# Kernel tuning notes

Hardware: AMD Instinct MI355X
Metric: run time of the kernel (lower is better)

## Reference

```python
import jax, jax.numpy as jnp
import numpy as np
from jax import lax

B, H, W, C, G, K = 2, 64, 64, 256, 8, 9
CQ = C // 4  # PConv partial channels
HC = C // G  # head channels
PTS = np.array([[-1, -1], [-1, 0], [-1, 1], [0, -1], [0, 0], [0, 1],
                [1, -1], [1, 0], [1, 1]], np.float32)  # (K,2) as (dx,dy)


def setup_inputs() -> dict:
    key = jax.random.key(0)
    ks = jax.random.split(key, 13)
    n = lambda i, shp, s: jax.random.normal(ks[i], shp, jnp.float32) * s
    return {
        'x': jax.random.normal(ks[0], (B, H, W, C), jnp.float32),
        'qkv_w': n(1, (C, 3 * C), C ** -0.5),
        'qkv_b': n(2, (3 * C,), 0.02),
        'dw_w': n(3, (3, 3, 1, 3 * C), 1.0 / 3.0),
        'dw_b': n(4, (3 * C,), 0.02),
        'off_pconv_w': n(5, (G, CQ, CQ, 3, 3), (CQ * 9) ** -0.5),
        'off_w': n(6, (G, 2 * K, C), 0.1 * C ** -0.5),
        'off_b': n(7, (G, 2 * K), 0.1),
        'mask_pconv_w': n(8, (CQ, CQ, 3, 3), (CQ * 9) ** -0.5),
        'mask_w': n(9, (K, C), C ** -0.5),
        'mask_b': n(10, (K,), 0.02),
        'proj_w': n(11, (C, C), C ** -0.5),
        'proj_b': n(12, (C,), 0.02),
    }


def _dwconv_nhwc(x, w, b):
    # depthwise 3x3, pad 1, stride 1; x (B,H,W,ch), w (3,3,1,ch)
    ch = x.shape[-1]
    y = lax.conv_general_dilated(x, w, (1, 1), 'SAME',
                                 dimension_numbers=('NHWC', 'HWIO', 'NHWC'),
                                 feature_group_count=ch)
    return y + b


def _pconv_nchw(x, w):
    # partial conv: 3x3 (no bias) on first CQ channels, rest untouched
    dc = w.shape[0]
    x1 = lax.conv_general_dilated(x[:, :dc], w, (1, 1), 'SAME',
                                  dimension_numbers=('NCHW', 'OIHW', 'NCHW'))
    return jnp.concatenate([x1, x[:, dc:]], axis=1)


def _flow_warp(x, flow):
    # x (N,Cc,Hh,Ww), flow (N,2K,Hh,Ww) -> (N,Cc,K,Hh,Ww)
    # bilinear grid_sample, border padding, align_corners=True == sampling at
    # absolute pixel coords with coordinate clamping.
    N, Cc, Hh, Ww = x.shape
    Kk = flow.shape[1] // 2
    fl = flow.reshape(N, Kk, 2, Hh, Ww).transpose(0, 3, 4, 1, 2)  # (N,H,W,K,2)
    gy, gx = jnp.meshgrid(jnp.arange(Hh, dtype=x.dtype),
                          jnp.arange(Ww, dtype=x.dtype), indexing='ij')
    base = jnp.stack([gx, gy], axis=-1)  # (H,W,2) in (x,y) order
    coords = base[None, :, :, None, :] + fl  # (N,H,W,K,2)
    cx = jnp.clip(coords[..., 0], 0.0, Ww - 1)
    cy = jnp.clip(coords[..., 1], 0.0, Hh - 1)
    x0 = jnp.floor(cx)
    y0 = jnp.floor(cy)
    wx = (cx - x0).reshape(N, 1, -1)
    wy = (cy - y0).reshape(N, 1, -1)
    x0i = x0.astype(jnp.int32)
    y0i = y0.astype(jnp.int32)
    x1i = jnp.minimum(x0i + 1, Ww - 1)
    y1i = jnp.minimum(y0i + 1, Hh - 1)
    xf = x.reshape(N, Cc, Hh * Ww)

    def gather(yi, xi):
        idx = (yi * Ww + xi).reshape(N, -1)  # (N, H*W*K)
        return jax.vmap(lambda im, ix: im[:, ix])(xf, idx)  # (N,Cc,H*W*K)

    v00 = gather(y0i, x0i)
    v01 = gather(y0i, x1i)
    v10 = gather(y1i, x0i)
    v11 = gather(y1i, x1i)
    out = (v00 * (1 - wx) * (1 - wy) + v01 * wx * (1 - wy)
           + v10 * (1 - wx) * wy + v11 * wx * wy)
    return out.reshape(N, Cc, Hh, Ww, Kk).transpose(0, 1, 4, 2, 3)


def reference(x, qkv_w, qkv_b, dw_w, dw_b, off_pconv_w, off_w, off_b,
              mask_pconv_w, mask_w, mask_b, proj_w, proj_b):
    Bb, Hh, Ww, Cc = x.shape
    P = Hh * Ww
    scale = HC ** -0.5
    # qkv projection + depthwise conv (NHWC)
    qkv = x @ qkv_w + qkv_b                       # (B,H,W,3C)
    qkv = _dwconv_nhwc(qkv, dw_w, dw_b)
    q = qkv[..., :Cc]                             # (B,H,W,C)
    k_map = jnp.transpose(qkv[..., Cc:2 * Cc], (0, 3, 1, 2))   # (B,C,H,W)
    v_map = jnp.transpose(qkv[..., 2 * Cc:], (0, 3, 1, 2))     # (B,C,H,W)
    q_nchw = jnp.transpose(q, (0, 3, 1, 2))

    # shared mask conv: PConv + 1x1 -> (B,K,H,W)
    xm = _pconv_nchw(q_nchw, mask_pconv_w)
    mask = jnp.einsum('bchw,oc->bohw', xm, mask_w) + mask_b[None, :, None, None]

    # base offsets per group: points_pool * (2g+1), flattened (dx,dy) pairs
    base = jnp.asarray(np.stack([(PTS * (2 * g + 1)).reshape(-1)
                                 for g in range(G)], axis=0))  # (G,2K)

    k_list, v_list = [], []
    for g in range(G):
        xo = _pconv_nchw(q_nchw, off_pconv_w[g])
        off = (jnp.einsum('bchw,oc->bohw', xo, off_w[g])
               + off_b[g][None, :, None, None]
               + base[g][None, :, None, None])  # (B,2K,H,W)
        sl = slice(g * HC, (g + 1) * HC)
        k_list.append(_flow_warp(k_map[:, sl], off) * mask[:, None])
        v_list.append(_flow_warp(v_map[:, sl], off) * mask[:, None])

    # stack (G,B,hc,K,H,W) -> (B,G,P,K,hc)
    def arrange(lst):
        t = jnp.stack(lst, axis=0).transpose(1, 0, 4, 5, 3, 2)
        return t.reshape(Bb, G, P, K, HC)

    k = arrange(k_list)
    v = arrange(v_list)
    qh = (q.reshape(Bb, Hh, Ww, G, HC).transpose(0, 3, 1, 2, 4)
          .reshape(Bb, G, P, HC)) * scale

    attn = jnp.einsum('bgpc,bgpkc->bgpk', qh, k)
    attn = jax.nn.softmax(attn, axis=-1)
    out = jnp.einsum('bgpk,bgpkc->bgpc', attn, v)       # (B,G,P,hc)
    out = out.transpose(0, 2, 1, 3).reshape(Bb, Hh, Ww, Cc)
    return out @ proj_w + proj_b
```

## Files before the change

### kernel.cpp

```cpp
#include <hip/hip_runtime.h>

typedef unsigned short u16;
typedef unsigned int u32;
typedef short bf16x8 __attribute__((ext_vector_type(8)));
typedef float f32x4 __attribute__((ext_vector_type(4)));
typedef float f32x2 __attribute__((ext_vector_type(2)));
typedef u32 u32x2 __attribute__((ext_vector_type(2)));

#define PP 4096
#define KPT 9

__device__ __forceinline__ u16 f2b(float f) {
    union { float f; unsigned int u; } v; v.f = f;
    unsigned int u = v.u;
    unsigned int r = u + 0x7FFFu + ((u >> 16) & 1u);
    return (u16)(r >> 16);
}
__device__ __forceinline__ float b2f(u16 b) {
    union { unsigned int u; float f; } v; v.u = ((unsigned int)b) << 16;
    return v.f;
}
__device__ __forceinline__ f32x2 unpk2(u32 u) {
    f32x2 r;
    r.x = __uint_as_float(u << 16);
    r.y = __uint_as_float(u & 0xFFFF0000u);
    return r;
}

__global__ __launch_bounds__(256) void prep_weights(
        const float* __restrict__ qkv_w, const float* __restrict__ proj_w,
        const float* __restrict__ off_pconv_w, const float* __restrict__ off_w,
        const float* __restrict__ off_b, const float* __restrict__ mask_pconv_w,
        const float* __restrict__ mask_w, const float* __restrict__ mask_b,
        u16* __restrict__ qkv_wT_b, u16* __restrict__ proj_wT_b,
        u16* __restrict__ cwT_b, float* __restrict__ cb) {
    int blk = blockIdx.x;
    if (blk < 1024) {
        int idx = blk * 256 + threadIdx.x;
        if (idx < 196608) {
            int r = idx / 768, c = idx % 768;
            qkv_wT_b[c * 256 + r] = f2b(qkv_w[idx]);
        } else {
            int i3 = idx - 196608;
            int r = i3 >> 8, c = i3 & 255;
            proj_wT_b[c * 256 + r] = f2b(proj_w[i3]);
        }
        return;
    }
    int k = blk - 1024;
    int o = threadIdx.x;
    if (o >= 160) return;
    float val = 0.f;
    if (o < 153) {
        if (k < 576) {
            int patch = k >> 6, i = k & 63;
            if (o < 144) {
                int g = o / 18, oo = o % 18;
                for (int c = 0; c < 64; c++)
                    val += off_w[(g * 18 + oo) * 256 + c] *
                           off_pconv_w[((g * 64 + c) * 64 + i) * 9 + patch];
            } else {
                int oo = o - 144;
                for (int c = 0; c < 64; c++)
                    val += mask_w[oo * 256 + c] * mask_pconv_w[(c * 64 + i) * 9 + patch];
            }
        } else {
            int j = k - 576;
            if (o < 144) {
                int g = o / 18, oo = o % 18;
                val = off_w[(g * 18 + oo) * 256 + 64 + j];
            } else {
                val = mask_w[(o - 144) * 256 + 64 + j];
            }
        }
    }
    cwT_b[o * 768 + k] = f2b(val);
    if (k == 0) {
        float bv = 0.f;
        if (o < 144) {
            int g = o / 18, oo = o % 18;
            const float PTSf[18] = {-1,-1,-1,0,-1,1,0,-1,0,0,0,1,1,-1,1,0,1,1};
            bv = off_b[g * 18 + oo] + PTSf[oo] * (float)(2 * g + 1);
        } else if (o < 153) {
            bv = mask_b[o - 144];
        }
        cb[o] = bv;
    }
}

template<bool OUT_BF16, bool A_F32, int KD>
__global__ __launch_bounds__(256) void mfma_gemm(
        const void* __restrict__ Av, const u16* __restrict__ BT,
        const float* __restrict__ bias, void* __restrict__ out, int N) {
    __shared__ u16 As[64][40];
    __shared__ u16 Bs[64][40];
    int tid = threadIdx.x;
    int row0 = blockIdx.x * 64, col0 = blockIdx.y * 64;
    int wid = tid >> 6, lane = tid & 63;
    int wr = wid >> 1, wc = wid & 1;
    int l15 = lane & 15, lhi = lane >> 4;
    f32x4 acc[2][2] = {};
    #pragma unroll
    for (int k0 = 0; k0 < KD; k0 += 32) {
        {
            int r = tid >> 2, kc = (tid & 3) * 8;
            if (A_F32) {
                const float* Af = (const float*)Av;
                f32x4 a0 = *(const f32x4*)&Af[(size_t)(row0 + r) * KD + k0 + kc];
                f32x4 a1 = *(const f32x4*)&Af[(size_t)(row0 + r) * KD + k0 + kc + 4];
                bf16x8 v;
                #pragma unroll
                for (int j = 0; j < 4; j++) { v[j] = (short)f2b(a0[j]); v[4+j] = (short)f2b(a1[j]); }
                *(bf16x8*)&As[r][kc] = v;
            } else {
                const u16* Ab = (const u16*)Av;
                *(bf16x8*)&As[r][kc] = *(const bf16x8*)&Ab[(size_t)(row0 + r) * KD + k0 + kc];
            }
            *(bf16x8*)&Bs[r][kc] = *(const bf16x8*)&BT[(size_t)(col0 + r) * KD + k0 + kc];
        }
        __syncthreads();
        bf16x8 bfr[2], afr[2];
        #pragma unroll
        for (int j = 0; j < 2; j++) {
            bfr[j] = *(const bf16x8*)&Bs[wc * 32 + j * 16 + l15][lhi * 8];
            afr[j] = *(const bf16x8*)&As[wr * 32 + j * 16 + l15][lhi * 8];
        }
        #pragma unroll
        for (int i = 0; i < 2; i++)
            #pragma unroll
            for (int j = 0; j < 2; j++)
                acc[i][j] = __builtin_amdgcn_mfma_f32_16x16x32_bf16(afr[i], bfr[j], acc[i][j], 0, 0, 0);
        __syncthreads();
    }
    #pragma unroll
    for (int i = 0; i < 2; i++) {
        int row = row0 + wr * 32 + i * 16 + lhi * 4;
        #pragma unroll
        for (int j = 0; j < 2; j++) {
            int col = col0 + wc * 32 + j * 16 + l15;
            float bv = bias[col];
            #pragma unroll
            for (int r = 0; r < 4; r++) {
                float v = acc[i][j][r] + bv;
                if (OUT_BF16) ((u16*)out)[(size_t)(row + r) * N + col] = f2b(v);
                else          ((float*)out)[(size_t)(row + r) * N + col] = v;
            }
        }
    }
}

__global__ __launch_bounds__(256) void dwconv_b(const u16* __restrict__ qkv_b,
        const float* __restrict__ dww, const float* __restrict__ dwb,
        u16* __restrict__ out) {
    int idx = blockIdx.x * 256 + threadIdx.x;
    int c8 = (idx % 96) * 8;
    int pix = idx / 96;
    int w = pix & 63, h = (pix >> 6) & 63, b = pix >> 12;
    float acc[8];
    #pragma unroll
    for (int j = 0; j < 8; j++) acc[j] = dwb[c8 + j];
    #pragma unroll
    for (int ky = 0; ky < 3; ky++) {
        int hh = h + ky - 1;
        if (hh < 0 || hh >= 64) continue;
        #pragma unroll
        for (int kx = 0; kx < 3; kx++) {
            int ww = w + kx - 1;
            if (ww < 0 || ww >= 64) continue;
            bf16x8 v = *(const bf16x8*)&qkv_b[((size_t)((b * 64 + hh) * 64 + ww)) * 768 + c8];
            #pragma unroll
            for (int j = 0; j < 8; j++)
                acc[j] += b2f((u16)v[j]) * dww[(ky * 3 + kx) * 768 + c8 + j];
        }
    }
    bf16x8 o;
    #pragma unroll
    for (int j = 0; j < 8; j++) o[j] = (short)f2b(acc[j]);
    *(bf16x8*)&out[(size_t)idx * 8] = o;
}

__global__ __launch_bounds__(256) void offmask_mfma(const u16* __restrict__ qdw_b,
        const u16* __restrict__ cwT_b, const float* __restrict__ cb,
        float* __restrict__ om0, float* __restrict__ om1,
        float* __restrict__ om2, float* __restrict__ om3) {
    __shared__ u16 As[32][40];
    __shared__ u16 Bs[160][40];
    int tid = threadIdx.x;
    int half = blockIdx.x & 3;
    int p0 = (blockIdx.x >> 2) * 32;
    int kbeg = half * 192;
    int kend = kbeg + 192;
    int wid = tid >> 6, lane = tid & 63;
    int wr = wid >> 1, wc = wid & 1;
    int l15 = lane & 15, lhi = lane >> 4;
    f32x4 acc[5] = {};
    for (int k0 = kbeg; k0 < kend; k0 += 32) {
        if (tid < 128) {
            int r = tid >> 2, kc = (tid & 3) * 8;
            int pixel = p0 + r;
            int w = pixel & 63, h = (pixel >> 6) & 63, b = pixel >> 12;
            bf16x8 v = {};
            if (k0 < 576) {
                int patch = k0 >> 6;
                int dy = patch / 3 - 1, dx = patch % 3 - 1;
                int hh = h + dy, ww = w + dx;
                if (hh >= 0 && hh < 64 && ww >= 0 && ww < 64)
                    v = *(const bf16x8*)&qdw_b[((size_t)((b * 64 + hh) * 64 + ww)) * 768 + (k0 & 63) + kc];
            } else {
                v = *(const bf16x8*)&qdw_b[((size_t)((b * 64 + h) * 64 + w)) * 768 + 64 + (k0 - 576) + kc];
            }
            *(bf16x8*)&As[r][kc] = v;
        }
        for (int idx = tid; idx < 640; idx += 256) {
            int r = idx >> 2, kc = (idx & 3) * 8;
            *(bf16x8*)&Bs[r][kc] = *(const bf16x8*)&cwT_b[r * 768 + k0 + kc];
        }
        __syncthreads();
        bf16x8 afr = *(const bf16x8*)&As[wr * 16 + l15][lhi * 8];
        #pragma unroll
        for (int j = 0; j < 5; j++) {
            bf16x8 bfr = *(const bf16x8*)&Bs[wc * 80 + j * 16 + l15][lhi * 8];
            acc[j] = __builtin_amdgcn_mfma_f32_16x16x32_bf16(afr, bfr, acc[j], 0, 0, 0);
        }
        __syncthreads();
    }
    float* dst = (half == 0) ? om0 : (half == 1) ? om1 : (half == 2) ? om2 : om3;
    int row = p0 + wr * 16 + lhi * 4;
    #pragma unroll
    for (int j = 0; j < 5; j++) {
        int col = wc * 80 + j * 16 + l15;
        float bv = (half == 0) ? cb[col] : 0.f;
        #pragma unroll
        for (int r = 0; r < 4; r++)
            dst[(size_t)(row + r) * 160 + col] = acc[j][r] + bv;
    }
}

__device__ __forceinline__ float4 pt_params(const float* __restrict__ om0,
        const float* __restrict__ om1, const float* __restrict__ om2,
        const float* __restrict__ om3, int pix, int g, int k) {
    int w = pix & 63, h = (pix >> 6) & 63;
    size_t rowb = (size_t)pix * 160;
    size_t db = rowb + g * 18 + 2 * k;
    f32x2 d0 = *(const f32x2*)&om0[db];
    f32x2 d1 = *(const f32x2*)&om1[db];
    f32x2 d2 = *(const f32x2*)&om2[db];
    f32x2 d3 = *(const f32x2*)&om3[db];
    float m = om0[rowb + 144 + k] + om1[rowb + 144 + k]
            + om2[rowb + 144 + k] + om3[rowb + 144 + k];
    float dx = d0.x + d1.x + d2.x + d3.x;
    float dy = d0.y + d1.y + d2.y + d3.y;
    float cx = fminf(fmaxf((float)w + dx, 0.f), 63.f);
    float cy = fminf(fmaxf((float)h + dy, 0.f), 63.f);
    float x0f = floorf(cx), y0f = floorf(cy);
    int x0 = (int)x0f, y0 = (int)y0f;
    u32 pk = (u32)((pix & ~4095) | (y0 << 6) | x0)
           | ((x0 < 63) ? 0x10000u : 0u) | ((y0 < 63) ? 0x20000u : 0u);
    float4 o;
    o.x = __uint_as_float(pk);
    o.y = cx - x0f;
    o.z = cy - y0f;
    o.w = m;
    return o;
}

__global__ __launch_bounds__(256) void deform_attn(const u16* __restrict__ qdw_b,
        const float* __restrict__ om0, const float* __restrict__ om1,
        const float* __restrict__ om2, const float* __restrict__ om3,
        u16* __restrict__ attn_b) {
    __shared__ float4 ptp[288];
    int tid = threadIdx.x;
    int bid = blockIdx.x;
    int sbid = (bid & 7) * 256 + (bid >> 3);
    for (int j = tid; j < 288; j += 256) {
        int u = j / 9, k = j % 9;
        int ppix = sbid * 4 + (u >> 3);
        ptp[j] = pt_params(om0, om1, om2, om3, ppix, u & 7, k);
    }
    __syncthreads();
    int t = tid >> 3;
    int cl = tid & 7;
    int g = t & 7;
    int pix = sbid * 4 + (t >> 3);
    const float scale = 0.17677669529663687f;
    int c0 = g * 32 + 4 * cl;
    u32x2 qu = *(const u32x2*)&qdw_b[(size_t)pix * 768 + c0];
    f32x2 qa = unpk2(qu.x) * scale;
    f32x2 qb = unpk2(qu.y) * scale;
    const char* base = (const char*)qdw_b;
    u32 ckb = (u32)(512 + c0 * 2);
    float logit[KPT];
    f32x2 va[KPT], vb[KPT];
    #pragma unroll
    for (int k_ = 0; k_ < KPT; k_++) {
        float4 q4 = ptp[t * 9 + k_];
        u32 pk = __float_as_uint(q4.x);
        float wx = q4.y, wy = q4.z, m = q4.w;
        u32 o00 = (pk & 0xFFFFu) * 1536u + ckb;
        u32 dX = (pk & 0x10000u) ? 1536u : 0u;
        u32 dY = (pk & 0x20000u) ? 98304u : 0u;
        u32 o01 = o00 + dX, o10 = o00 + dY, o11 = o00 + dY + dX;
        u32x2 K00 = *(const u32x2*)(base + o00);
        u32x2 V00 = *(const u32x2*)(base + o00 + 512);
        u32x2 K01 = *(const u32x2*)(base + o01);
        u32x2 V01 = *(const u32x2*)(base + o01 + 512);
        u32x2 K10 = *(const u32x2*)(base + o10);
        u32x2 V10 = *(const u32x2*)(base + o10 + 512);
        u32x2 K11 = *(const u32x2*)(base + o11);
        u32x2 V11 = *(const u32x2*)(base + o11 + 512);
        float w00 = (1.f - wx) * (1.f - wy), w01 = wx * (1.f - wy);
        float w10 = (1.f - wx) * wy,         w11 = wx * wy;
        f32x2 ka = unpk2(K00.x) * w00 + unpk2(K01.x) * w01
                 + unpk2(K10.x) * w10 + unpk2(K11.x) * w11;
        f32x2 kb = unpk2(K00.y) * w00 + unpk2(K01.y) * w01
                 + unpk2(K10.y) * w10 + unpk2(K11.y) * w11;
        f32x2 vva = unpk2(V00.x) * w00 + unpk2(V01.x) * w01
                  + unpk2(V10.x) * w10 + unpk2(V11.x) * w11;
        f32x2 vvb = unpk2(V00.y) * w00 + unpk2(V01.y) * w01
                  + unpk2(V10.y) * w10 + unpk2(V11.y) * w11;
        f32x2 pr = qa * ka + qb * kb;
        float part = pr.x + pr.y;
        part += __shfl_xor(part, 4);
        part += __shfl_xor(part, 2);
        part += __shfl_xor(part, 1);
        logit[k_] = part * m;
        va[k_] = vva * m;
        vb[k_] = vvb * m;
    }
    float mx = fmaxf(fmaxf(fmaxf(logit[0], logit[1]), fmaxf(logit[2], logit[3])),
                     fmaxf(fmaxf(logit[4], logit[5]),
                           fmaxf(fmaxf(logit[6], logit[7]), logit[8])));
    float s = 0.f;
    #pragma unroll
    for (int k_ = 0; k_ < KPT; k_++) { logit[k_] = __expf(logit[k_] - mx); s += logit[k_]; }
    float inv = 1.f / s;
    f32x2 oa = {0.f, 0.f}, ob = {0.f, 0.f};
    #pragma unroll
    for (int k_ = 0; k_ < KPT; k_++) { oa += va[k_] * logit[k_]; ob += vb[k_] * logit[k_]; }
    oa *= inv; ob *= inv;
    u32x2 outw;
    outw.x = (u32)f2b(oa.x) | ((u32)f2b(oa.y) << 16);
    outw.y = (u32)f2b(ob.x) | ((u32)f2b(ob.y) << 16);
    *(u32x2*)&attn_b[(size_t)pix * 256 + c0] = outw;
}

extern "C" void kernel_launch(void* const* d_in, const int* in_sizes, int n_in,
                              void* d_out, int out_size, void* d_ws, size_t ws_size,
                              hipStream_t stream) {
    const float* x            = (const float*)d_in[0];
    const float* qkv_w        = (const float*)d_in[1];
    const float* qkv_b        = (const float*)d_in[2];
    const float* dw_w         = (const float*)d_in[3];
    const float* dw_b         = (const float*)d_in[4];
    const float* off_pconv_w  = (const float*)d_in[5];
    const float* off_w        = (const float*)d_in[6];
    const float* off_b        = (const float*)d_in[7];
    const float* mask_pconv_w = (const float*)d_in[8];
    const float* mask_w       = (const float*)d_in[9];
    const float* mask_b       = (const float*)d_in[10];
    const float* proj_w       = (const float*)d_in[11];
    const float* proj_b       = (const float*)d_in[12];

    char* ws = (char*)d_ws;
    size_t off = 0;
    u16*   qkv_wT_b   = (u16*)(ws + off);                 off += 768ull*256*2;
    u16*   proj_wT_b  = (u16*)(ws + off);                 off += 256ull*256*2;
    u16*   qkv_bf     = (u16*)(ws + off);                 off += 8192ull*768*2;
    u16*   qdw_b      = (u16*)(ws + off);                 off += 8192ull*768*2;
    u16*   cwT_b      = (u16*)(ws + off);                 off += 160ull*768*2;
    float* cb         = (float*)(ws + off);               off += 256*4;
    float* om0        = (float*)(ws + off);               off += 8192ull*160*4;
    float* om1        = (float*)(ws + off);               off += 8192ull*160*4;
    float* om2        = (float*)(ws + off);               off += 8192ull*160*4;
    float* om3        = (float*)(ws + off);               off += 8192ull*160*4;
    u16*   attn_b     = (u16*)(ws + off);                 off += 8192ull*256*2;

    prep_weights<<<1792, 256, 0, stream>>>(qkv_w, proj_w, off_pconv_w, off_w, off_b,
                                           mask_pconv_w, mask_w, mask_b,
                                           qkv_wT_b, proj_wT_b, cwT_b, cb);
    mfma_gemm<true, true, 256><<<dim3(128, 12), 256, 0, stream>>>(x, qkv_wT_b, qkv_b,
                                                                  qkv_bf, 768);
    dwconv_b<<<3072, 256, 0, stream>>>(qkv_bf, dw_w, dw_b, qdw_b);
    offmask_mfma<<<1024, 256, 0, stream>>>(qdw_b, cwT_b, cb, om0, om1, om2, om3);
    deform_attn<<<2048, 256, 0, stream>>>(qdw_b, om0, om1, om2, om3, attn_b);
    mfma_gemm<false, false, 256><<<dim3(128, 4), 256, 0, stream>>>(attn_b, proj_wT_b,
                                                                   proj_b, d_out, 256);
}
```

Before: 162.8 us.

## Fuse output projection GEMM into deformable attention kernel epilogue

```diff
diff --git a/kernel.cpp b/kernel.cpp
--- a/kernel.cpp
+++ b/kernel.cpp
@@ -267,8 +267,10 @@
 __global__ __launch_bounds__(256) void deform_attn(const u16* __restrict__ qdw_b,
         const float* __restrict__ om0, const float* __restrict__ om1,
         const float* __restrict__ om2, const float* __restrict__ om3,
-        u16* __restrict__ attn_b) {
+        const u16* __restrict__ projT, const float* __restrict__ proj_b,
+        float* __restrict__ outp) {
     __shared__ float4 ptp[288];
+    __shared__ u16 att_lds[4][264];
     int tid = threadIdx.x;
     int bid = blockIdx.x;
     int sbid = (bid & 7) * 256 + (bid >> 3);
@@ -281,7 +283,8 @@
     int t = tid >> 3;
     int cl = tid & 7;
     int g = t & 7;
-    int pix = sbid * 4 + (t >> 3);
+    int prow = t >> 3;
+    int pix = sbid * 4 + prow;
     const float scale = 0.17677669529663687f;
     int c0 = g * 32 + 4 * cl;
     u32x2 qu = *(const u32x2*)&qdw_b[(size_t)pix * 768 + c0];
@@ -338,10 +341,35 @@
     #pragma unroll
     for (int k_ = 0; k_ < KPT; k_++) { oa += va[k_] * logit[k_]; ob += vb[k_] * logit[k_]; }
     oa *= inv; ob *= inv;
-    u32x2 outw;
-    outw.x = (u32)f2b(oa.x) | ((u32)f2b(oa.y) << 16);
-    outw.y = (u32)f2b(ob.x) | ((u32)f2b(ob.y) << 16);
-    *(u32x2*)&attn_b[(size_t)pix * 256 + c0] = outw;
+    att_lds[prow][c0 + 0] = f2b(oa.x);
+    att_lds[prow][c0 + 1] = f2b(oa.y);
+    att_lds[prow][c0 + 2] = f2b(ob.x);
+    att_lds[prow][c0 + 3] = f2b(ob.y);
+    __syncthreads();
+    int wid = tid >> 6, lane = tid & 63;
+    int l15 = lane & 15, lhi = lane >> 4;
+    f32x4 pacc[4] = {};
+    #pragma unroll
+    for (int k0 = 0; k0 < 8; k0++) {
+        bf16x8 afr = {};
+        if (l15 < 4) afr = *(const bf16x8*)&att_lds[l15][k0 * 32 + lhi * 8];
+        #pragma unroll
+        for (int n16 = 0; n16 < 4; n16++) {
+            int ncol = wid * 64 + n16 * 16 + l15;
+            bf16x8 bfr = *(const bf16x8*)&projT[(size_t)ncol * 256 + k0 * 32 + lhi * 8];
+            pacc[n16] = __builtin_amdgcn_mfma_f32_16x16x32_bf16(afr, bfr, pacc[n16], 0, 0, 0);
+        }
+    }
+    if (lhi == 0) {
+        #pragma unroll
+        for (int n16 = 0; n16 < 4; n16++) {
+            int ncol = wid * 64 + n16 * 16 + l15;
+            float bv = proj_b[ncol];
+            #pragma unroll
+            for (int r = 0; r < 4; r++)
+                outp[(size_t)(sbid * 4 + r) * 256 + ncol] = pacc[n16][r] + bv;
+        }
+    }
 }
 
 extern "C" void kernel_launch(void* const* d_in, const int* in_sizes, int n_in,
@@ -373,7 +401,6 @@
     float* om1        = (float*)(ws + off);               off += 8192ull*160*4;
     float* om2        = (float*)(ws + off);               off += 8192ull*160*4;
     float* om3        = (float*)(ws + off);               off += 8192ull*160*4;
-    u16*   attn_b     = (u16*)(ws + off);                 off += 8192ull*256*2;
 
     prep_weights<<<1792, 256, 0, stream>>>(qkv_w, proj_w, off_pconv_w, off_w, off_b,
                                            mask_pconv_w, mask_w, mask_b,
@@ -382,7 +409,6 @@
                                                                   qkv_bf, 768);
     dwconv_b<<<3072, 256, 0, stream>>>(qkv_bf, dw_w, dw_b, qdw_b);
     offmask_mfma<<<1024, 256, 0, stream>>>(qdw_b, cwT_b, cb, om0, om1, om2, om3);
-    deform_attn<<<2048, 256, 0, stream>>>(qdw_b, om0, om1, om2, om3, attn_b);
-    mfma_gemm<false, false, 256><<<dim3(128, 4), 256, 0, stream>>>(attn_b, proj_wT_b,
-                                                                   proj_b, d_out, 256);
-}
+    deform_attn<<<2048, 256, 0, stream>>>(qdw_b, om0, om1, om2, om3,
+                                          proj_wT_b, proj_b, (float*)d_out);
+}
```

Result: slower. 184.3 us (+13.3%).
